# Optimization experiments

Measured on AMD Instinct MI355X. Metric: run time of the kernel, lower is better.

Reference implementation:

```python
import jax, jax.numpy as jnp
import numpy as np

N = 100_000          # nodes
E = 3_200_000        # edges (avg degree 32)
NEG_SLOPE = 0.2      # PyG GATConv default


def _gat_conv(x, src, dst, W, a_src, a_dst, b, n):
    """Single-head PyG-style GATConv. src/dst already include self-loops."""
    h = x @ W                                   # [N, F_out]
    logits = (h @ a_src)[src] + (h @ a_dst)[dst]  # [E']
    e = jax.nn.leaky_relu(logits, NEG_SLOPE)
    m = jax.ops.segment_max(e, dst, num_segments=n)
    ex = jnp.exp(e - m[dst])                    # stable ragged softmax over in-edges
    s = jax.ops.segment_sum(ex, dst, num_segments=n)
    alpha = ex / (s[dst] + 1e-16)
    out = jax.ops.segment_sum(h[src] * alpha[:, None], dst, num_segments=n)
    return out + b


def setup_inputs() -> dict:
    key = jax.random.key(0)
    ks = jax.random.split(key, 20)
    x = jax.random.normal(ks[0], (N, 3), dtype=jnp.float32)
    edge_index = jax.random.randint(ks[1], (2, E), 0, N, dtype=jnp.int64)

    def lin(k, fin, fout):
        return jax.random.normal(k, (fin, fout), dtype=jnp.float32) * (1.0 / np.sqrt(fin))

    def att(k, f):
        return jax.random.normal(k, (f,), dtype=jnp.float32) * (1.0 / np.sqrt(f))

    inp = {"x": x, "edge_index": edge_index}
    # forward-direction convs
    inp["W1"], inp["as1"], inp["ad1"], inp["b1"] = lin(ks[2], 3, 16), att(ks[3], 16), att(ks[4], 16), jnp.zeros((16,), jnp.float32)
    inp["W2"], inp["as2"], inp["ad2"], inp["b2"] = lin(ks[5], 16, 1), att(ks[6], 1), att(ks[7], 1), jnp.zeros((1,), jnp.float32)
    # reverse-direction convs
    inp["W1r"], inp["as1r"], inp["ad1r"], inp["b1r"] = lin(ks[8], 3, 16), att(ks[9], 16), att(ks[10], 16), jnp.zeros((16,), jnp.float32)
    inp["W2r"], inp["as2r"], inp["ad2r"], inp["b2r"] = lin(ks[11], 16, 1), att(ks[12], 1), att(ks[13], 1), jnp.zeros((1,), jnp.float32)
    return inp


def reference(x, edge_index, W1, as1, ad1, b1, W2, as2, ad2, b2,
              W1r, as1r, ad1r, b1r, W2r, as2r, ad2r, b2r):
    n = x.shape[0]
    loops = jnp.arange(n, dtype=edge_index.dtype)
    # forward direction (self-loops appended, as PyG add_self_loops=True)
    src = jnp.concatenate([edge_index[0], loops])
    dst = jnp.concatenate([edge_index[1], loops])
    # reverse direction: stack([ei[1], ei[0]]) then self-loops
    rsrc = jnp.concatenate([edge_index[1], loops])
    rdst = jnp.concatenate([edge_index[0], loops])

    xf = jax.nn.relu(_gat_conv(x, src, dst, W1, as1, ad1, b1, n))
    xf = _gat_conv(xf, src, dst, W2, as2, ad2, b2, n)

    xr = jax.nn.relu(_gat_conv(x, rsrc, rdst, W1r, as1r, ad1r, b1r, n))
    xr = _gat_conv(xr, rsrc, rdst, W2r, as2r, ad2r, b2r, n)

    return (xf + xr) * 0.5
```

## Files before the change

kernel.cpp:

```cpp
#include <hip/hip_runtime.h>
#include <math.h>

#define NSLOPE 0.2f
#define BSH 8
#define BNODES 256
#define NID_MASK 0x1FFFF
#define SENT 0xFFFFFFFFu
#define CAP 10240
#define GB 768
#define RE 2560
#define EPT 5
#define SLOT 12
#define SPILLCAP 256
#define BN9 512
#define LCAP 18432
#define BAGT 1024
#define CPP9 9

__device__ __forceinline__ float lrelu(float v) { return v > 0.f ? v : NSLOPE * v; }

__global__ void k_prep(const float* __restrict__ x,
                       const float* __restrict__ as1, const float* __restrict__ ad1,
                       const float* __restrict__ as1r, const float* __restrict__ ad1r,
                       const float* __restrict__ W1, const float* __restrict__ W1r,
                       float4* __restrict__ rec4f, float4* __restrict__ rec4r,
                       float* __restrict__ s1df, float* __restrict__ s1dr,
                       int* __restrict__ gcur, int NS, int N) {
    int i = blockIdx.x * blockDim.x + threadIdx.x;
    if (i < NS) gcur[i] = 0;
    if (i >= N) return;
    float x0 = x[3 * i], x1 = x[3 * i + 1], x2 = x[3 * i + 2];
    float ssf = 0.f, sdf = 0.f, ssr = 0.f, sdr = 0.f;
#pragma unroll
    for (int k = 0; k < 16; k++) {
        float hf = x0 * W1[k] + x1 * W1[16 + k] + x2 * W1[32 + k];
        ssf += hf * as1[k];
        sdf += hf * ad1[k];
        float hr = x0 * W1r[k] + x1 * W1r[16 + k] + x2 * W1r[32 + k];
        ssr += hr * as1r[k];
        sdr += hr * ad1r[k];
    }
    rec4f[i] = make_float4(x0, x1, x2, ssf);
    rec4r[i] = make_float4(x0, x1, x2, ssr);
    s1df[i] = sdf; s1dr[i] = sdr;
}

__global__ void __launch_bounds__(512) k_scatsort(
        const void* __restrict__ ei, long long E,
        int NB, int NS, int* __restrict__ gcur, unsigned* __restrict__ bin) {
    extern __shared__ unsigned smem[];
    unsigned* slots = smem;
    int* cnt  = (int*)(slots + (size_t)NS * SLOT);
    int* gpos = cnt + NS;
    int* spill_s = gpos + NS;
    int* spill_p = spill_s + SPILLCAP;
    unsigned* spill_r = (unsigned*)(spill_p + SPILLCAP);
    int* spn = (int*)(spill_r + SPILLCAP);
    __shared__ int flagsm;

    int t = threadIdx.x;
    if (t < 64) {
        const unsigned long long* p = (const unsigned long long*)ei;
        bool bad = false;
#pragma unroll
        for (int i = 0; i < 4; i++)
            if (p[t * 4 + i] >= (1ull << 32)) bad = true;
        unsigned long long mask = __ballot(bad);
        if (t == 0) flagsm = (mask == 0ull) ? 1 : 0;
    }
    __syncthreads();
    int fl = flagsm;
    long long chunk = (E + GB - 1) / GB;
    long long cstart = (long long)blockIdx.x * chunk;
    long long cend = cstart + chunk; if (cend > E) cend = E;

    for (long long rs = cstart; rs < cend; rs += RE) {
        int ne = (int)min((long long)RE, cend - rs);
        for (int c = t; c < NS; c += 512) cnt[c] = 0;
        if (t == 0) *spn = 0;
        int eu[EPT], ev[EPT];
#pragma unroll
        for (int k = 0; k < EPT; k++) {
            int idx = t + k * 512;
            eu[k] = -1;
            if (idx < ne) {
                long long i = rs + idx;
                if (fl) { const long long* p = (const long long*)ei;
                          eu[k] = (int)p[i]; ev[k] = (int)p[E + i]; }
                else    { const int* p = (const int*)ei;
                          eu[k] = p[i]; ev[k] = p[E + i]; }
            }
        }
        __syncthreads();
#pragma unroll
        for (int k = 0; k < EPT; k++) {
            if (eu[k] >= 0) {
                int u = eu[k], v = ev[k];
                unsigned r0 = (unsigned)u | ((unsigned)(v & (BNODES - 1)) << 17);
                int s0 = v >> BSH;
                unsigned r1 = (unsigned)v | ((unsigned)(u & (BNODES - 1)) << 17);
                int s1 = NB + (u >> BSH);
                int p0 = atomicAdd(&cnt[s0], 1);
                if (p0 < SLOT) slots[s0 * SLOT + p0] = r0;
                else { int sp = atomicAdd(spn, 1); if (sp < SPILLCAP) { spill_s[sp] = s0; spill_p[sp] = p0; spill_r[sp] = r0; } }
                int p1 = atomicAdd(&cnt[s1], 1);
                if (p1 < SLOT) slots[s1 * SLOT + p1] = r1;
                else { int sp = atomicAdd(spn, 1); if (sp < SPILLCAP) { spill_s[sp] = s1; spill_p[sp] = p1; spill_r[sp] = r1; } }
            }
        }
        __syncthreads();
        for (int c = t; c < NS; c += 512) {
            int n = cnt[c];
            gpos[c] = n ? atomicAdd(&gcur[c], n) : 0;
        }
        __syncthreads();
        for (int c = t; c < NS; c += 512) {
            int n = cnt[c];
            if (!n) continue;
            int g = gpos[c];
            long long b = (long long)c * CAP;
            int m = n < SLOT ? n : SLOT;
            if (g + n <= CAP) {
                int j = 0;
                if (g & 1) { bin[b + g] = slots[c * SLOT]; j = 1; }
                for (; j + 2 <= m; j += 2)
                    *(uint2*)(bin + b + g + j) =
                        make_uint2(slots[c * SLOT + j], slots[c * SLOT + j + 1]);
                if (j < m) bin[b + g + j] = slots[c * SLOT + j];
            }
        }
        int nsp = *spn; if (nsp > SPILLCAP) nsp = SPILLCAP;
        for (int i = t; i < nsp; i += 512) {
            int s = spill_s[i];
            int off = gpos[s] + spill_p[i];
            if (off < CAP) bin[(long long)s * CAP + off] = spill_r[i];
        }
        __syncthreads();
    }
}

__global__ void __launch_bounds__(BAGT, 8) k_bagg1(
        unsigned* __restrict__ bin, const int* __restrict__ gcur,
        const float4* __restrict__ rec4f, const float* __restrict__ s1df,
        const float4* __restrict__ rec4r, const float* __restrict__ s1dr,
        const float* __restrict__ b1, const float* __restrict__ W1,
        const float* __restrict__ W2,
        const float* __restrict__ as2, const float* __restrict__ ad2,
        const float* __restrict__ b1r, const float* __restrict__ W1r,
        const float* __restrict__ W2r,
        const float* __restrict__ as2r, const float* __restrict__ ad2r,
        float2* __restrict__ p2f, float* __restrict__ s2df,
        float2* __restrict__ p2r, float* __restrict__ s2dr,
        int* __restrict__ aoff, int* __restrict__ aend, int NB8, int N) {
    int bb = blockIdx.x, dir = blockIdx.y;
    const float4* rec4 = dir ? rec4r : rec4f;
    const float* s1d = dir ? s1dr : s1df;
    const float* b1_ = dir ? b1r : b1;
    const float* W1_ = dir ? W1r : W1;
    const float* W2_ = dir ? W2r : W2;
    float as2v = dir ? as2r[0] : as2[0];
    float ad2v = dir ? ad2r[0] : ad2[0];
    float2* p2 = dir ? p2r : p2f;
    float* s2d = dir ? s2dr : s2df;

    int c0 = dir * NB8 + 2 * bb;
    bool c1ok = (2 * bb + 1) < NB8;
    long long base = (long long)c0 * CAP;
    int n0 = gcur[c0]; if (n0 > CAP) n0 = CAP;
    int n1 = c1ok ? gcur[c0 + 1] : 0; if (n1 > CAP) n1 = CAP;
    int np0 = (n0 + 1) >> 1, np1 = (n1 + 1) >> 1;
    if (np0 > LCAP / 2) np0 = LCAP / 2;
    if (np0 + np1 > LCAP / 2) np1 = LCAP / 2 - np0;
    int nptot = np0 + np1;
    int v0 = bb << 9;
    int nv = N - v0; if (nv > BN9) nv = BN9;

    __shared__ int cnt[BN9];
    __shared__ int loff[BN9];
    __shared__ int segtot[8];
    __shared__ unsigned lds_u[LCAP];
    int t = threadIdx.x;

    const uint2* bp0 = (const uint2*)(bin + base);
    const uint2* bp1 = (const uint2*)(bin + base) + CAP / 2;
    uint2 recs[CPP9];
#pragma unroll
    for (int k = 0; k < CPP9; k++) {
        int i = t + k * BAGT;
        uint2 r = make_uint2(SENT, SENT);
        if (i < np0) {
            r = bp0[i];
            if (2 * i + 1 >= n0) r.y = SENT;
        } else if (i < nptot) {
            int i1 = i - np0;
            r = bp1[i1];
            if (2 * i1 + 1 >= n1) r.y = SENT;
            r.x += (256u << 17);
            if (r.y != SENT) r.y += (256u << 17);
        }
        recs[k] = r;
    }
    if (t < BN9) cnt[t] = 0;
    __syncthreads();
#pragma unroll
    for (int k = 0; k < CPP9; k++) {
        if (recs[k].x != SENT) atomicAdd(&cnt[recs[k].x >> 17], 1);
        if (recs[k].y != SENT) atomicAdd(&cnt[recs[k].y >> 17], 1);
    }
    __syncthreads();
    if (t < BN9) {
        int lane = t & 63, wv = t >> 6;
        int val = cnt[t];
        int incl = val;
#pragma unroll
        for (int od = 1; od < 64; od <<= 1) {
            int up = __shfl_up(incl, od);
            if (lane >= od) incl += up;
        }
        if (lane == 63) segtot[wv] = incl;
        loff[t] = incl - val;
    }
    __syncthreads();
    if (t < BN9) {
        int wv = t >> 6;
        int offs = 0;
#pragma unroll
        for (int j = 0; j < 8; j++) offs += (j < wv) ? segtot[j] : 0;
        int ex = loff[t] + offs;
        loff[t] = ex;
        cnt[t] = ex;
    }
    __syncthreads();
#pragma unroll
    for (int k = 0; k < CPP9; k++) {
        if (recs[k].x != SENT) {
            int p = atomicAdd(&cnt[recs[k].x >> 17], 1);
            lds_u[p] = recs[k].x & NID_MASK;
        }
        if (recs[k].y != SENT) {
            int p = atomicAdd(&cnt[recs[k].y >> 17], 1);
            lds_u[p] = recs[k].y & NID_MASK;
        }
    }
    __syncthreads();
    int node = t >> 1, lane = t & 1;
    float sdv = (node < nv) ? s1d[v0 + node] : 0.f;
    float d = 0.f, a0 = 0.f, a1 = 0.f, a2 = 0.f;
    if (node < nv) {
        int ls = loff[node], le = cnt[node];
        for (int pos = ls + lane; pos < le; pos += 2) {
            unsigned u = lds_u[pos];
            float4 r = rec4[u];
            float w = __expf(lrelu(r.w + sdv));
            d += w; a0 += w * r.x; a1 += w * r.y; a2 += w * r.z;
        }
    }
    d  += __shfl_xor(d, 1);
    a0 += __shfl_xor(a0, 1);
    a1 += __shfl_xor(a1, 1);
    a2 += __shfl_xor(a2, 1);
    if (lane == 0 && node < nv) {
        int v = v0 + node;
        float4 r = rec4[v];
        float w = __expf(lrelu(r.w + sdv));
        float dd = d + w;
        float inv = 1.f / (dd + 1e-16f);
        float m0 = (a0 + w * r.x) * inv;
        float m1 = (a1 + w * r.y) * inv;
        float m2 = (a2 + w * r.z) * inv;
        float h2v = 0.f;
#pragma unroll
        for (int k = 0; k < 16; k++) {
            float o = m0 * W1_[k] + m1 * W1_[16 + k] + m2 * W1_[32 + k] + b1_[k];
            o = fmaxf(o, 0.f);
            h2v += o * W2_[k];
        }
        p2[v] = make_float2(h2v, h2v * as2v);
        s2d[v] = h2v * ad2v;
    }
    int nreal = (nv > 0) ? cnt[nv - 1] : 0;
    if (t == 0 && (nreal & 1)) lds_u[nreal] = SENT;
    __syncthreads();
    int ndp = (nreal + 1) >> 1;
    uint2* bq = (uint2*)(bin + base);
    for (int i = t; i < ndp; i += BAGT)
        bq[i] = make_uint2(lds_u[2 * i], lds_u[2 * i + 1]);
    if (t < nv) {
        aoff[dir * N + v0 + t] = (int)(base + loff[t]);
        aend[dir * N + v0 + t] = (int)(base + cnt[t]);
    }
}

__global__ void k_agg2(const unsigned* __restrict__ bin,
                       const int* __restrict__ aoff, const int* __restrict__ aend,
                       const float2* __restrict__ p2f, const float* __restrict__ s2df,
                       const float2* __restrict__ p2r, const float* __restrict__ s2dr,
                       const float* __restrict__ b2, const float* __restrict__ b2r,
                       float* __restrict__ out, int N) {
    int tid = blockIdx.x * blockDim.x + threadIdx.x;
    int v = tid >> 4;
    int lane = tid & 15;
    if (v >= N) return;
    float res[2];
#pragma unroll
    for (int dir = 0; dir < 2; dir++) {
        const float2* p2 = dir ? p2r : p2f;
        const float* s2d = dir ? s2dr : s2df;
        float bias = dir ? b2r[0] : b2[0];
        float sd = s2d[v];
        int st = aoff[dir * N + v], en = aend[dir * N + v];
        float d = 0.f, a = 0.f;
        if (lane == 0) {
            float2 ts = p2[v];
            float w = __expf(lrelu(ts.y + sd));
            d = w; a = w * ts.x;
        }
        int j = st + lane;
        for (; j + 16 < en; j += 32) {
            unsigned u0 = __builtin_nontemporal_load(bin + j);
            unsigned u1 = __builtin_nontemporal_load(bin + j + 16);
            float2 t0 = p2[u0];
            float2 t1 = p2[u1];
            float w0 = __expf(lrelu(t0.y + sd));
            float w1 = __expf(lrelu(t1.y + sd));
            d += w0 + w1;
            a += w0 * t0.x + w1 * t1.x;
        }
        for (; j < en; j += 16) {
            unsigned u = __builtin_nontemporal_load(bin + j);
            float2 t = p2[u];
            float w = __expf(lrelu(t.y + sd));
            d += w;
            a += w * t.x;
        }
#pragma unroll
        for (int mask = 1; mask < 16; mask <<= 1) {
            d += __shfl_xor(d, mask);
            a += __shfl_xor(a, mask);
        }
        res[dir] = a / (d + 1e-16f) + bias;
    }
    if (lane == 0) out[v] = 0.5f * (res[0] + res[1]);
}

extern "C" void kernel_launch(void* const* d_in, const int* in_sizes, int n_in,
                              void* d_out, int out_size, void* d_ws, size_t ws_size,
                              hipStream_t stream) {
    const float* x   = (const float*)d_in[0];
    const void*  ei  = d_in[1];
    const float* W1  = (const float*)d_in[2];
    const float* as1 = (const float*)d_in[3];
    const float* ad1 = (const float*)d_in[4];
    const float* b1  = (const float*)d_in[5];
    const float* W2  = (const float*)d_in[6];
    const float* as2 = (const float*)d_in[7];
    const float* ad2 = (const float*)d_in[8];
    const float* b2  = (const float*)d_in[9];
    const float* W1r  = (const float*)d_in[10];
    const float* as1r = (const float*)d_in[11];
    const float* ad1r = (const float*)d_in[12];
    const float* b1r  = (const float*)d_in[13];
    const float* W2r  = (const float*)d_in[14];
    const float* as2r = (const float*)d_in[15];
    const float* ad2r = (const float*)d_in[16];
    const float* b2r  = (const float*)d_in[17];

    const int N = in_sizes[0] / 3;
    const long long E = in_sizes[1] / 2;
    const int NB8 = (N + BNODES - 1) >> BSH;
    const int NS = 2 * NB8;
    const int NB9 = (N + BN9 - 1) >> 9;

    char* w = (char*)d_ws;
    size_t o = 0;
    auto A = [&](size_t bytes) { o = (o + 255) & ~(size_t)255; size_t r = o; o += bytes; return r; };
    size_t oR4f  = A(sizeof(float4) * N);
    size_t oR4r  = A(sizeof(float4) * N);
    size_t oS1df = A(sizeof(float) * N);
    size_t oS1dr = A(sizeof(float) * N);
    size_t oP2f  = A(sizeof(float2) * N);
    size_t oS2df = A(sizeof(float) * N);
    size_t oP2r  = A(sizeof(float2) * N);
    size_t oS2dr = A(sizeof(float) * N);
    size_t oAoff = A(sizeof(int) * 2 * N);
    size_t oAend = A(sizeof(int) * 2 * N);
    size_t oGcur = A(sizeof(int) * NS);
    size_t oBin  = A(sizeof(unsigned) * (size_t)NS * CAP);
    (void)ws_size; (void)n_in; (void)out_size;

    float4* rec4f = (float4*)(w + oR4f);
    float4* rec4r = (float4*)(w + oR4r);
    float*  s1df = (float*)(w + oS1df);
    float*  s1dr = (float*)(w + oS1dr);
    float2* p2f  = (float2*)(w + oP2f);
    float*  s2df = (float*)(w + oS2df);
    float2* p2r  = (float2*)(w + oP2r);
    float*  s2dr = (float*)(w + oS2dr);
    int*    aoff = (int*)(w + oAoff);
    int*    aend = (int*)(w + oAend);
    int*    gcur = (int*)(w + oGcur);
    unsigned* bin = (unsigned*)(w + oBin);

    dim3 gN((N + 255) / 256);
    dim3 gAgg1(NB9, 2);
    dim3 gAgg2((N * 16 + 255) / 256);

    size_t smem = sizeof(unsigned) * (size_t)NS * SLOT
                + sizeof(int) * (size_t)NS * 2
                + sizeof(int) * SPILLCAP * 2
                + sizeof(unsigned) * SPILLCAP
                + 64;

    k_prep<<<gN, 256, 0, stream>>>(x, as1, ad1, as1r, ad1r, W1, W1r,
                                   rec4f, rec4r, s1df, s1dr, gcur, NS, N);
    k_scatsort<<<GB, 512, smem, stream>>>(ei, E, NB8, NS, gcur, bin);
    k_bagg1<<<gAgg1, BAGT, 0, stream>>>(bin, gcur, rec4f, s1df, rec4r, s1dr,
                                        b1, W1, W2, as2, ad2,
                                        b1r, W1r, W2r, as2r, ad2r,
                                        p2f, s2df, p2r, s2dr, aoff, aend, NB8, N);
    k_agg2<<<gAgg2, 256, 0, stream>>>(bin, aoff, aend, p2f, s2df, p2r, s2dr,
                                      b2, b2r, (float*)d_out, N);
}
```

Baseline: 235.2 us.

## Fuse scatter-sort, layer-1 and layer-2 aggregation into one cooperative kernel

```diff
diff --git a/kernel.cpp b/kernel.cpp
--- a/kernel.cpp
+++ b/kernel.cpp
@@ -1,5 +1,8 @@
 #include <hip/hip_runtime.h>
+#include <hip/hip_cooperative_groups.h>
 #include <math.h>
+
+namespace cg = cooperative_groups;
 
 #define NSLOPE 0.2f
 #define BSH 8
@@ -7,15 +10,21 @@
 #define NID_MASK 0x1FFFF
 #define SENT 0xFFFFFFFFu
 #define CAP 10240
+#define NSMAX 800
+#define BN9 512
+#define LCAP 17408
+#define CPP9 9
+#define TPB 1024
+#define FRE 5120
+#define FEPT 5
+#define FSLOT 20
+#define FSPILL 256
+#define AUXN (2 * NSMAX + 3 * FSPILL + 2)
 #define GB 768
 #define RE 2560
 #define EPT 5
 #define SLOT 12
 #define SPILLCAP 256
-#define BN9 512
-#define LCAP 18432
-#define BAGT 1024
-#define CPP9 9
 
 __device__ __forceinline__ float lrelu(float v) { return v > 0.f ? v : NSLOPE * v; }
 
@@ -43,6 +52,278 @@
     rec4f[i] = make_float4(x0, x1, x2, ssf);
     rec4r[i] = make_float4(x0, x1, x2, ssr);
     s1df[i] = sdf; s1dr[i] = sdr;
+}
+
+struct FP {
+    const void* ei; long long E;
+    int NB8, NS, N;
+    int* gcur; unsigned* bin;
+    const float4* rec4f; const float* s1df;
+    const float4* rec4r; const float* s1dr;
+    const float *b1, *W1, *W2, *as2, *ad2;
+    const float *b1r, *W1r, *W2r, *as2r, *ad2r;
+    const float *b2, *b2r;
+    float2 *p2f, *p2r; float *s2df, *s2dr;
+    float* res; float* out;
+};
+
+__global__ void __launch_bounds__(TPB, 8) k_fused(FP p) {
+    cg::grid_group grid = cg::this_grid();
+    __shared__ unsigned s_big[LCAP];
+    __shared__ int s_aux[AUXN];
+    __shared__ int flagsm;
+    int t = threadIdx.x;
+    int bid = blockIdx.x;
+    int GRID = gridDim.x;
+
+    {
+        unsigned* strips = s_big;
+        int* scnt  = s_aux;
+        int* sgpos = s_aux + NSMAX;
+        int* sps   = s_aux + 2 * NSMAX;
+        int* spp   = sps + FSPILL;
+        unsigned* spr = (unsigned*)(spp + FSPILL);
+        int* spn   = (int*)(spr + FSPILL);
+
+        if (t < 64) {
+            const unsigned long long* q = (const unsigned long long*)p.ei;
+            bool bad = false;
+#pragma unroll
+            for (int i = 0; i < 4; i++)
+                if (q[t * 4 + i] >= (1ull << 32)) bad = true;
+            unsigned long long mask = __ballot(bad);
+            if (t == 0) flagsm = (mask == 0ull) ? 1 : 0;
+        }
+        __syncthreads();
+        int fl = flagsm;
+        long long chunk = (p.E + GRID - 1) / GRID;
+        long long cstart = (long long)bid * chunk;
+        long long cend = cstart + chunk; if (cend > p.E) cend = p.E;
+
+        for (long long rs = cstart; rs < cend; rs += FRE) {
+            int ne = (int)min((long long)FRE, cend - rs);
+            for (int c = t; c < p.NS; c += TPB) scnt[c] = 0;
+            if (t == 0) *spn = 0;
+            int eu[FEPT], ev[FEPT];
+#pragma unroll
+            for (int k = 0; k < FEPT; k++) {
+                int idx = t + k * TPB;
+                eu[k] = -1;
+                if (idx < ne) {
+                    long long i = rs + idx;
+                    if (fl) { const long long* q = (const long long*)p.ei;
+                              eu[k] = (int)q[i]; ev[k] = (int)q[p.E + i]; }
+                    else    { const int* q = (const int*)p.ei;
+                              eu[k] = q[i]; ev[k] = q[p.E + i]; }
+                }
+            }
+            __syncthreads();
+#pragma unroll
+            for (int k = 0; k < FEPT; k++) {
+                if (eu[k] >= 0) {
+                    int u = eu[k], v = ev[k];
+                    unsigned r0 = (unsigned)u | ((unsigned)(v & (BNODES - 1)) << 17);
+                    int s0 = v >> BSH;
+                    unsigned r1 = (unsigned)v | ((unsigned)(u & (BNODES - 1)) << 17);
+                    int s1 = p.NB8 + (u >> BSH);
+                    int p0 = atomicAdd(&scnt[s0], 1);
+                    if (p0 < FSLOT) strips[s0 * FSLOT + p0] = r0;
+                    else { int sp = atomicAdd(spn, 1); if (sp < FSPILL) { sps[sp] = s0; spp[sp] = p0; spr[sp] = r0; } }
+                    int p1 = atomicAdd(&scnt[s1], 1);
+                    if (p1 < FSLOT) strips[s1 * FSLOT + p1] = r1;
+                    else { int sp = atomicAdd(spn, 1); if (sp < FSPILL) { sps[sp] = s1; spp[sp] = p1; spr[sp] = r1; } }
+                }
+            }
+            __syncthreads();
+            for (int c = t; c < p.NS; c += TPB) {
+                int n = scnt[c];
+                sgpos[c] = n ? atomicAdd(&p.gcur[c], n) : 0;
+            }
+            __syncthreads();
+            for (int c = t; c < p.NS; c += TPB) {
+                int n = scnt[c];
+                if (!n) continue;
+                int g = sgpos[c];
+                long long b = (long long)c * CAP;
+                int m = n < FSLOT ? n : FSLOT;
+                if (g + n <= CAP) {
+                    int j = 0;
+                    if (g & 1) { p.bin[b + g] = strips[c * FSLOT]; j = 1; }
+                    for (; j + 2 <= m; j += 2)
+                        *(uint2*)(p.bin + b + g + j) =
+                            make_uint2(strips[c * FSLOT + j], strips[c * FSLOT + j + 1]);
+                    if (j < m) p.bin[b + g + j] = strips[c * FSLOT + j];
+                }
+            }
+            int nsp = *spn; if (nsp > FSPILL) nsp = FSPILL;
+            for (int i = t; i < nsp; i += TPB) {
+                int s = sps[i];
+                int off = sgpos[s] + spp[i];
+                if (off < CAP) p.bin[(long long)s * CAP + off] = spr[i];
+            }
+            __syncthreads();
+        }
+    }
+    __threadfence();
+    grid.sync();
+
+    unsigned* lds_u = s_big;
+    int* cnt  = s_aux;
+    int* loff = s_aux + BN9;
+    int* segtot = s_aux + 2 * BN9;
+
+    int dir = bid & 1, bb = bid >> 1;
+    const float4* rec4 = dir ? p.rec4r : p.rec4f;
+    const float* s1d = dir ? p.s1dr : p.s1df;
+    const float* b1_ = dir ? p.b1r : p.b1;
+    const float* W1_ = dir ? p.W1r : p.W1;
+    const float* W2_ = dir ? p.W2r : p.W2;
+    float as2v = dir ? p.as2r[0] : p.as2[0];
+    float ad2v = dir ? p.ad2r[0] : p.ad2[0];
+    float2* p2 = dir ? p.p2r : p.p2f;
+    float* s2d = dir ? p.s2dr : p.s2df;
+
+    int c0 = dir * p.NB8 + 2 * bb;
+    bool c1ok = (2 * bb + 1) < p.NB8;
+    long long base = (long long)c0 * CAP;
+    int n0 = p.gcur[c0]; if (n0 > CAP) n0 = CAP;
+    int n1 = c1ok ? p.gcur[c0 + 1] : 0; if (n1 > CAP) n1 = CAP;
+    int np0 = (n0 + 1) >> 1, np1 = (n1 + 1) >> 1;
+    if (np0 > LCAP / 2) np0 = LCAP / 2;
+    if (np0 + np1 > LCAP / 2) np1 = LCAP / 2 - np0;
+    int nptot = np0 + np1;
+    int v0 = bb << 9;
+    int nv = p.N - v0; if (nv > BN9) nv = BN9;
+
+    const uint2* bp0 = (const uint2*)(p.bin + base);
+    const uint2* bp1 = (const uint2*)(p.bin + base) + CAP / 2;
+    uint2 recs[CPP9];
+#pragma unroll
+    for (int k = 0; k < CPP9; k++) {
+        int i = t + k * TPB;
+        uint2 r = make_uint2(SENT, SENT);
+        if (i < np0) {
+            r = bp0[i];
+            if (2 * i + 1 >= n0) r.y = SENT;
+        } else if (i < nptot) {
+            int i1 = i - np0;
+            r = bp1[i1];
+            if (2 * i1 + 1 >= n1) r.y = SENT;
+            r.x += (256u << 17);
+            if (r.y != SENT) r.y += (256u << 17);
+        }
+        recs[k] = r;
+    }
+    if (t < BN9) cnt[t] = 0;
+    __syncthreads();
+#pragma unroll
+    for (int k = 0; k < CPP9; k++) {
+        if (recs[k].x != SENT) atomicAdd(&cnt[recs[k].x >> 17], 1);
+        if (recs[k].y != SENT) atomicAdd(&cnt[recs[k].y >> 17], 1);
+    }
+    __syncthreads();
+    if (t < BN9) {
+        int lane = t & 63, wv = t >> 6;
+        int val = cnt[t];
+        int incl = val;
+#pragma unroll
+        for (int od = 1; od < 64; od <<= 1) {
+            int up = __shfl_up(incl, od);
+            if (lane >= od) incl += up;
+        }
+        if (lane == 63) segtot[wv] = incl;
+        loff[t] = incl - val;
+    }
+    __syncthreads();
+    if (t < BN9) {
+        int wv = t >> 6;
+        int offs = 0;
+#pragma unroll
+        for (int j = 0; j < 8; j++) offs += (j < wv) ? segtot[j] : 0;
+        int ex = loff[t] + offs;
+        loff[t] = ex;
+        cnt[t] = ex;
+    }
+    __syncthreads();
+#pragma unroll
+    for (int k = 0; k < CPP9; k++) {
+        if (recs[k].x != SENT) {
+            int q = atomicAdd(&cnt[recs[k].x >> 17], 1);
+            lds_u[q] = recs[k].x & NID_MASK;
+        }
+        if (recs[k].y != SENT) {
+            int q = atomicAdd(&cnt[recs[k].y >> 17], 1);
+            lds_u[q] = recs[k].y & NID_MASK;
+        }
+    }
+    __syncthreads();
+    int node = t >> 1, lane = t & 1;
+    float sdv = (node < nv) ? s1d[v0 + node] : 0.f;
+    {
+        float d = 0.f, a0 = 0.f, a1 = 0.f, a2 = 0.f;
+        if (node < nv) {
+            int ls = loff[node], le = cnt[node];
+            for (int pos = ls + lane; pos < le; pos += 2) {
+                unsigned u = lds_u[pos];
+                float4 r = rec4[u];
+                float w = __expf(lrelu(r.w + sdv));
+                d += w; a0 += w * r.x; a1 += w * r.y; a2 += w * r.z;
+            }
+        }
+        d  += __shfl_xor(d, 1);
+        a0 += __shfl_xor(a0, 1);
+        a1 += __shfl_xor(a1, 1);
+        a2 += __shfl_xor(a2, 1);
+        if (lane == 0 && node < nv) {
+            int v = v0 + node;
+            float4 r = rec4[v];
+            float w = __expf(lrelu(r.w + sdv));
+            float dd = d + w;
+            float inv = 1.f / (dd + 1e-16f);
+            float m0 = (a0 + w * r.x) * inv;
+            float m1 = (a1 + w * r.y) * inv;
+            float m2 = (a2 + w * r.z) * inv;
+            float h2v = 0.f;
+#pragma unroll
+            for (int k = 0; k < 16; k++) {
+                float o = m0 * W1_[k] + m1 * W1_[16 + k] + m2 * W1_[32 + k] + b1_[k];
+                o = fmaxf(o, 0.f);
+                h2v += o * W2_[k];
+            }
+            p2[v] = make_float2(h2v, h2v * as2v);
+            s2d[v] = h2v * ad2v;
+        }
+    }
+    __threadfence();
+    grid.sync();
+
+    {
+        float bias = dir ? p.b2r[0] : p.b2[0];
+        float sd2 = (node < nv) ? s2d[v0 + node] : 0.f;
+        float d = 0.f, a = 0.f;
+        if (node < nv) {
+            int ls = loff[node], le = cnt[node];
+            for (int pos = ls + lane; pos < le; pos += 2) {
+                unsigned u = lds_u[pos];
+                float2 r = p2[u];
+                float w = __expf(lrelu(r.y + sd2));
+                d += w; a += w * r.x;
+            }
+        }
+        d += __shfl_xor(d, 1);
+        a += __shfl_xor(a, 1);
+        if (lane == 0 && node < nv) {
+            int v = v0 + node;
+            float2 r = p2[v];
+            float w = __expf(lrelu(r.y + sd2));
+            p.res[dir * p.N + v] = (a + w * r.x) / (d + w + 1e-16f) + bias;
+        }
+    }
+    __threadfence();
+    grid.sync();
+
+    for (int i = bid * TPB + t; i < p.N; i += GRID * TPB)
+        p.out[i] = 0.5f * (p.res[i] + p.res[p.N + i]);
 }
 
 __global__ void __launch_bounds__(512) k_scatsort(
@@ -139,7 +420,7 @@
     }
 }
 
-__global__ void __launch_bounds__(BAGT, 8) k_bagg1(
+__global__ void __launch_bounds__(TPB, 8) k_bagg1(
         unsigned* __restrict__ bin, const int* __restrict__ gcur,
         const float4* __restrict__ rec4f, const float* __restrict__ s1df,
         const float4* __restrict__ rec4r, const float* __restrict__ s1dr,
@@ -186,7 +467,7 @@
     uint2 recs[CPP9];
 #pragma unroll
     for (int k = 0; k < CPP9; k++) {
-        int i = t + k * BAGT;
+        int i = t + k * TPB;
         uint2 r = make_uint2(SENT, SENT);
         if (i < np0) {
             r = bp0[i];
@@ -234,12 +515,12 @@
 #pragma unroll
     for (int k = 0; k < CPP9; k++) {
         if (recs[k].x != SENT) {
-            int p = atomicAdd(&cnt[recs[k].x >> 17], 1);
-            lds_u[p] = recs[k].x & NID_MASK;
+            int q = atomicAdd(&cnt[recs[k].x >> 17], 1);
+            lds_u[q] = recs[k].x & NID_MASK;
         }
         if (recs[k].y != SENT) {
-            int p = atomicAdd(&cnt[recs[k].y >> 17], 1);
-            lds_u[p] = recs[k].y & NID_MASK;
+            int q = atomicAdd(&cnt[recs[k].y >> 17], 1);
+            lds_u[q] = recs[k].y & NID_MASK;
         }
     }
     __syncthreads();
@@ -283,7 +564,7 @@
     __syncthreads();
     int ndp = (nreal + 1) >> 1;
     uint2* bq = (uint2*)(bin + base);
-    for (int i = t; i < ndp; i += BAGT)
+    for (int i = t; i < ndp; i += TPB)
         bq[i] = make_uint2(lds_u[2 * i], lds_u[2 * i + 1]);
     if (t < nv) {
         aoff[dir * N + v0 + t] = (int)(base + loff[t]);
@@ -382,6 +663,7 @@
     size_t oS2df = A(sizeof(float) * N);
     size_t oP2r  = A(sizeof(float2) * N);
     size_t oS2dr = A(sizeof(float) * N);
+    size_t oRes  = A(sizeof(float) * 2 * N);
     size_t oAoff = A(sizeof(int) * 2 * N);
     size_t oAend = A(sizeof(int) * 2 * N);
     size_t oGcur = A(sizeof(int) * NS);
@@ -396,28 +678,43 @@
     float*  s2df = (float*)(w + oS2df);
     float2* p2r  = (float2*)(w + oP2r);
     float*  s2dr = (float*)(w + oS2dr);
+    float*  res  = (float*)(w + oRes);
     int*    aoff = (int*)(w + oAoff);
     int*    aend = (int*)(w + oAend);
     int*    gcur = (int*)(w + oGcur);
     unsigned* bin = (unsigned*)(w + oBin);
 
     dim3 gN((N + 255) / 256);
-    dim3 gAgg1(NB9, 2);
-    dim3 gAgg2((N * 16 + 255) / 256);
-
-    size_t smem = sizeof(unsigned) * (size_t)NS * SLOT
-                + sizeof(int) * (size_t)NS * 2
-                + sizeof(int) * SPILLCAP * 2
-                + sizeof(unsigned) * SPILLCAP
-                + 64;
 
     k_prep<<<gN, 256, 0, stream>>>(x, as1, ad1, as1r, ad1r, W1, W1r,
                                    rec4f, rec4r, s1df, s1dr, gcur, NS, N);
-    k_scatsort<<<GB, 512, smem, stream>>>(ei, E, NB8, NS, gcur, bin);
-    k_bagg1<<<gAgg1, BAGT, 0, stream>>>(bin, gcur, rec4f, s1df, rec4r, s1dr,
-                                        b1, W1, W2, as2, ad2,
-                                        b1r, W1r, W2r, as2r, ad2r,
-                                        p2f, s2df, p2r, s2dr, aoff, aend, NB8, N);
-    k_agg2<<<gAgg2, 256, 0, stream>>>(bin, aoff, aend, p2f, s2df, p2r, s2dr,
-                                      b2, b2r, (float*)d_out, N);
+
+    FP p;
+    p.ei = ei; p.E = E; p.NB8 = NB8; p.NS = NS; p.N = N;
+    p.gcur = gcur; p.bin = bin;
+    p.rec4f = rec4f; p.s1df = s1df; p.rec4r = rec4r; p.s1dr = s1dr;
+    p.b1 = b1; p.W1 = W1; p.W2 = W2; p.as2 = as2; p.ad2 = ad2;
+    p.b1r = b1r; p.W1r = W1r; p.W2r = W2r; p.as2r = as2r; p.ad2r = ad2r;
+    p.b2 = b2; p.b2r = b2r;
+    p.p2f = p2f; p.p2r = p2r; p.s2df = s2df; p.s2dr = s2dr;
+    p.res = res; p.out = (float*)d_out;
+
+    void* args[] = { &p };
+    hipError_t cerr = hipLaunchCooperativeKernel((const void*)k_fused,
+                                                 dim3(2 * NB9), dim3(TPB),
+                                                 args, 0, stream);
+    if (cerr != hipSuccess) {
+        size_t smem = sizeof(unsigned) * (size_t)NS * SLOT
+                    + sizeof(int) * (size_t)NS * 2
+                    + sizeof(int) * SPILLCAP * 2
+                    + sizeof(unsigned) * SPILLCAP
+                    + 64;
+        k_scatsort<<<GB, 512, smem, stream>>>(ei, E, NB8, NS, gcur, bin);
+        k_bagg1<<<dim3(NB9, 2), TPB, 0, stream>>>(bin, gcur, rec4f, s1df, rec4r, s1dr,
+                                                  b1, W1, W2, as2, ad2,
+                                                  b1r, W1r, W2r, as2r, ad2r,
+                                                  p2f, s2df, p2r, s2dr, aoff, aend, NB8, N);
+        k_agg2<<<dim3((N * 16 + 255) / 256), 256, 0, stream>>>(
+            bin, aoff, aend, p2f, s2df, p2r, s2dr, b2, b2r, (float*)d_out, N);
+    }
 }
```

Result: slower. 788.0 us (+235.0%).
